# Kernel tuning notes

Hardware: AMD Instinct MI355X
Metric: run time of the kernel (lower is better)

## Reference

```python
import jax, jax.numpy as jnp
import numpy as np

N_NODES = 100000
N_EDGES = 1000000
D_FEAT = 64
N_FILTER = 64
N_CLASSES = 16


def gcn_norm(edge_idx, n):
    """Add self-loops and compute symmetric normalization D^-1/2 (A+I) D^-1/2."""
    loop = jnp.arange(n, dtype=edge_idx.dtype)
    src = jnp.concatenate([edge_idx[0], loop])  # [E+N]
    dst = jnp.concatenate([edge_idx[1], loop])  # [E+N]
    w = jnp.ones(src.shape[0], dtype=jnp.float32)
    deg = jax.ops.segment_sum(w, dst, num_segments=n)  # in-degree incl. self-loop
    dinv = jnp.where(deg > 0, jax.lax.rsqrt(deg), 0.0)
    norm = dinv[src] * w * dinv[dst]  # [E+N]
    return src, dst, norm


def gcn_conv(x, W, b, src, dst, norm, n):
    h = x @ W                                   # [n, f] dense transform first (f <= d)
    msg = h[src] * norm[:, None]                # gather + scale  [E+N, f]
    out = jax.ops.segment_sum(msg, dst, num_segments=n)  # scatter-add  [n, f]
    return out + b


def setup_inputs() -> dict:
    key = jax.random.key(0)
    k1, k2, k3, k4 = jax.random.split(key, 4)
    X = jax.random.normal(k1, (N_NODES, D_FEAT), dtype=jnp.float32)
    edge_idx = jax.random.randint(k2, (2, N_EDGES), 0, N_NODES, dtype=jnp.int64)
    W1 = jax.random.normal(k3, (D_FEAT, N_FILTER), dtype=jnp.float32) * 0.05
    b1 = jnp.zeros((N_FILTER,), dtype=jnp.float32)
    W2 = jax.random.normal(k4, (N_FILTER, N_CLASSES), dtype=jnp.float32) * 0.05
    b2 = jnp.zeros((N_CLASSES,), dtype=jnp.float32)
    return {"X": X, "edge_idx": edge_idx, "W1": W1, "b1": b1, "W2": W2, "b2": b2}


def reference(X, edge_idx, W1, b1, W2, b2):
    n = X.shape[0]
    src, dst, norm = gcn_norm(edge_idx, n)
    x = gcn_conv(X, W1, b1, src, dst, norm, n)
    x = jax.nn.relu(x)
    # dropout p=0 -> identity
    x = gcn_conv(x, W2, b2, src, dst, norm, n)
    return x  # raw logits; pred_layer is not applied in the torch forward
```

## Files before the change

kernel.cpp:

```cpp
#include <hip/hip_runtime.h>
#include <hip/hip_bf16.h>


constexpr int N = 100000;
constexpr int E = 1000000;
constexpr int NB = (N + 511) / 512;
constexpr int CAP = 6144;
constexpr int CSTRIDE = 32;
constexpr int CHUNK = 2048;
constexpr int NBLK = (E + CHUNK - 1) / CHUNK;
constexpr int BT = 512;
constexpr int BTF = 1024;
constexpr int NPW = 3;
constexpr int NW = (N + NPW - 1) / NPW;
constexpr int NWBLK = (NW + 3) / 4;

__device__ __forceinline__ float bflo(unsigned u) { return __uint_as_float(u << 16); }
__device__ __forceinline__ float bfhi(unsigned u) { return __uint_as_float(u & 0xffff0000u); }

__device__ __forceinline__ void wait_lgkm0() {
    __builtin_amdgcn_s_waitcnt(0xc07f);
    __builtin_amdgcn_sched_barrier(0);
}

__global__ void k_bfill(const int* __restrict__ src, const int* __restrict__ dst,
                        int* __restrict__ cursor, int* __restrict__ bkt) {
    __shared__ int hist[256];
    __shared__ int lbase[256];
    __shared__ int gbase[256];
    __shared__ int lcur[256];
    __shared__ int ws[8];
    __shared__ int stage[CHUNK];
    __shared__ unsigned char sbkt[CHUNK];
    int t = threadIdx.x;
    int lane = t & 63;
    int e0 = blockIdx.x * CHUNK;
    int cnt = min(CHUNK, E - e0);

    if (t < 256) hist[t] = 0;
    __syncthreads();
    for (int j = t; j < cnt; j += BT)
        atomicAdd(&hist[dst[e0 + j] >> 9], 1);
    __syncthreads();
    int h = (t < 256) ? hist[t] : 0;
    int v = h;
#pragma unroll
    for (int off = 1; off < 64; off <<= 1) {
        int u = __shfl_up(v, off);
        if (lane >= off) v += u;
    }
    if (lane == 63) ws[t >> 6] = v;
    __syncthreads();
    int add = 0;
    for (int i = 0; i < (t >> 6); ++i) add += ws[i];
    int inc = v + add;
    if (t < 256) { lbase[t] = inc - h; lcur[t] = 0; }
    if (t < NB) gbase[t] = h ? atomicAdd(&cursor[t * CSTRIDE], h) : 0;
    __syncthreads();
    for (int j = t; j < cnt; j += BT) {
        int d = dst[e0 + j];
        int b = d >> 9;
        int pos = lbase[b] + atomicAdd(&lcur[b], 1);
        stage[pos] = ((d & 511) << 17) | src[e0 + j];
        sbkt[pos] = (unsigned char)b;
    }
    __syncthreads();
    for (int j = t; j < cnt; j += BT) {
        int b = sbkt[j];
        int gpos = gbase[b] + (j - lbase[b]);
        if (gpos < CAP) bkt[b * CAP + gpos] = stage[j];
    }
}

__global__ void k_bfine(const int* __restrict__ cursor, const int* __restrict__ bkt,
                        int* __restrict__ row_ptr, float* __restrict__ dinv,
                        int* __restrict__ csr_src) {
    __shared__ int cnt[512];
    __shared__ int excl[512];
    __shared__ int ws[16];
    int b = blockIdx.x;
    int t = threadIdx.x;
    int lane = t & 63;
    int c = (t < NB) ? cursor[t * CSTRIDE] : 0;
    int mv = (t < b) ? c : 0;
#pragma unroll
    for (int off = 1; off < 64; off <<= 1) mv += __shfl_xor(mv, off);
    if (lane == 0) ws[t >> 6] = mv;
    if (t < 512) cnt[t] = 0;
    __syncthreads();
    int base = 0;
#pragma unroll
    for (int i = 0; i < 16; ++i) base += ws[i];
    int m = cursor[b * CSTRIDE];
    if (b == 0 && t == 0) row_ptr[N] = E;
    const int* bb = bkt + b * CAP;
    const int4* bb4 = (const int4*)bb;
    int m4 = m >> 2;
    for (int j = t; j < m4; j += BTF) {
        int4 v = bb4[j];
        atomicAdd(&cnt[v.x >> 17], 1); atomicAdd(&cnt[v.y >> 17], 1);
        atomicAdd(&cnt[v.z >> 17], 1); atomicAdd(&cnt[v.w >> 17], 1);
    }
    for (int j = (m4 << 2) + t; j < m; j += BTF) atomicAdd(&cnt[bb[j] >> 17], 1);
    __syncthreads();
    if (t < 512) {
        int h = cnt[t];
        int v = h;
#pragma unroll
        for (int off = 1; off < 64; off <<= 1) {
            int u = __shfl_up(v, off);
            if (lane >= off) v += u;
        }
        if (lane == 63) ws[t >> 6] = v;
        excl[t] = v - h;
    }
    __syncthreads();
    if (t < 512) {
        int add = 0;
        for (int i = 0; i < (t >> 6); ++i) add += ws[i];
        int ex = excl[t] + add;
        excl[t] = ex;
        int node = b * 512 + t;
        if (node < N) {
            row_ptr[node] = base + ex;
            dinv[node] = rsqrtf((float)(cnt[t] + 1));
        }
    }
    __syncthreads();
    for (int j = t; j < m4; j += BTF) {
        int4 v4 = bb4[j];
        int p0 = atomicAdd(&excl[v4.x >> 17], 1); csr_src[base + p0] = v4.x & 0x1FFFF;
        int p1 = atomicAdd(&excl[v4.y >> 17], 1); csr_src[base + p1] = v4.y & 0x1FFFF;
        int p2 = atomicAdd(&excl[v4.z >> 17], 1); csr_src[base + p2] = v4.z & 0x1FFFF;
        int p3 = atomicAdd(&excl[v4.w >> 17], 1); csr_src[base + p3] = v4.w & 0x1FFFF;
    }
    for (int j = (m4 << 2) + t; j < m; j += BTF) {
        int vv = bb[j];
        int p = atomicAdd(&excl[vv >> 17], 1);
        csr_src[base + p] = vv & 0x1FFFF;
    }
}

__global__ void k_gemm1(const float* __restrict__ X, const float* __restrict__ W1,
                        const float* __restrict__ dinv, __hip_bfloat16* __restrict__ h1s,
                        __hip_bfloat16* __restrict__ h2s) {
    __shared__ float sX[4][4][64];
    int t = threadIdx.x;
    int lane = t & 63;
    int w = t >> 6;
    int wid = (blockIdx.x * 256 + t) >> 6;
    if (blockIdx.x == 0) {
        if (t < 64) h1s[(size_t)N * 64 + t] = __float2bfloat16(0.f);
        if (t < 16) h2s[(size_t)N * 16 + t] = __float2bfloat16(0.f);
    }
    float w1[64];
#pragma unroll
    for (int k = 0; k < 64; ++k) w1[k] = W1[k * 64 + lane];
    constexpr int STRIDE = 4096 * 4;
    int r4 = wid * 4;
    float x0 = X[(size_t)r4 * 64 + lane];
    float x1 = X[(size_t)(r4 + 1) * 64 + lane];
    float x2 = X[(size_t)(r4 + 2) * 64 + lane];
    float x3 = X[(size_t)(r4 + 3) * 64 + lane];
    for (; r4 < N; r4 += STRIDE) {
        int rn = r4 + STRIDE;
        float y0 = 0.f, y1 = 0.f, y2 = 0.f, y3 = 0.f;
        if (rn < N) {
            y0 = X[(size_t)rn * 64 + lane];
            y1 = X[(size_t)(rn + 1) * 64 + lane];
            y2 = X[(size_t)(rn + 2) * 64 + lane];
            y3 = X[(size_t)(rn + 3) * 64 + lane];
        }
        float dv0 = dinv[r4], dv1 = dinv[r4 + 1], dv2 = dinv[r4 + 2], dv3 = dinv[r4 + 3];
        sX[w][0][lane] = x0; sX[w][1][lane] = x1;
        sX[w][2][lane] = x2; sX[w][3][lane] = x3;
        wait_lgkm0();
        float acc0 = 0.f, acc1 = 0.f, acc2 = 0.f, acc3 = 0.f;
#pragma unroll
        for (int k = 0; k < 64; ++k) {
            float wk = w1[k];
            acc0 = fmaf(sX[w][0][k], wk, acc0);
            acc1 = fmaf(sX[w][1][k], wk, acc1);
            acc2 = fmaf(sX[w][2][k], wk, acc2);
            acc3 = fmaf(sX[w][3][k], wk, acc3);
        }
        acc0 *= dv0; acc1 *= dv1; acc2 *= dv2; acc3 *= dv3;
        float up0 = __shfl_xor(acc0, 1);
        float up1 = __shfl_xor(acc1, 1);
        float up2 = __shfl_xor(acc2, 1);
        float up3 = __shfl_xor(acc3, 1);
        if (!(lane & 1)) {
            __hip_bfloat162 p;
            p.x = __float2bfloat16(acc0); p.y = __float2bfloat16(up0);
            *(__hip_bfloat162*)(h1s + (size_t)r4 * 64 + lane) = p;
            p.x = __float2bfloat16(acc1); p.y = __float2bfloat16(up1);
            *(__hip_bfloat162*)(h1s + (size_t)(r4 + 1) * 64 + lane) = p;
            p.x = __float2bfloat16(acc2); p.y = __float2bfloat16(up2);
            *(__hip_bfloat162*)(h1s + (size_t)(r4 + 2) * 64 + lane) = p;
            p.x = __float2bfloat16(acc3); p.y = __float2bfloat16(up3);
            *(__hip_bfloat162*)(h1s + (size_t)(r4 + 3) * 64 + lane) = p;
        }
        x0 = y0; x1 = y1; x2 = y2; x3 = y3;
    }
}

__global__ void k_layer12(const int* __restrict__ row_ptr, const int* __restrict__ csr_src,
                          const float* __restrict__ dinv, const __hip_bfloat16* __restrict__ h1s,
                          const float* __restrict__ b1, const float* __restrict__ W2,
                          __hip_bfloat16* __restrict__ h2s) {
    __shared__ float sy[4][8][72];
    int t = threadIdx.x;
    int lane = t & 63;
    int w = t >> 6;
    int g8 = lane >> 3;
    int qo = (lane & 7) << 4;
    int g16 = lane >> 4, c16 = lane & 15;
    int wid = blockIdx.x * 4 + w;
    int d0 = wid * NPW;
    if (d0 >= N) return;
    int dend = min(d0 + NPW, N);
    float w2[16];
#pragma unroll
    for (int j = 0; j < 16; ++j) w2[j] = W2[(g16 * 16 + j) * 16 + c16];
    float b1v = b1[lane];
    const char* Hb = (const char*)h1s;

    int rp0 = row_ptr[d0];
    for (int d = d0; d < dend; ++d) {
        int rp1 = row_ptr[d + 1];
        float dv = dinv[d];
        float a[8] = {0, 0, 0, 0, 0, 0, 0, 0};
        if (g8 == 0) {
            uint4 u = *(const uint4*)(Hb + (((unsigned)d << 7) | qo));
            a[0] = bflo(u.x); a[1] = bfhi(u.x); a[2] = bflo(u.y); a[3] = bfhi(u.y);
            a[4] = bflo(u.z); a[5] = bfhi(u.z); a[6] = bflo(u.w); a[7] = bfhi(u.w);
        }
        for (int base = rp0; base < rp1; base += 64) {
            int nloc = min(64, rp1 - base);
            int sidx = (lane < nloc) ? csr_src[base + lane] : N;
            int steps = (nloc + 15) >> 4;
            for (int j = 0; j < steps; ++j) {
                int b0 = (j << 4) | g8;
                int s0 = __shfl(sidx, b0);
                int s1 = __shfl(sidx, b0 | 8);
                uint4 u0 = *(const uint4*)(Hb + (((unsigned)s0 << 7) | qo));
                uint4 u1 = *(const uint4*)(Hb + (((unsigned)s1 << 7) | qo));
                a[0] += bflo(u0.x); a[1] += bfhi(u0.x); a[2] += bflo(u0.y); a[3] += bfhi(u0.y);
                a[4] += bflo(u0.z); a[5] += bfhi(u0.z); a[6] += bflo(u0.w); a[7] += bfhi(u0.w);
                a[0] += bflo(u1.x); a[1] += bfhi(u1.x); a[2] += bflo(u1.y); a[3] += bfhi(u1.y);
                a[4] += bflo(u1.z); a[5] += bfhi(u1.z); a[6] += bflo(u1.w); a[7] += bfhi(u1.w);
            }
        }
        rp0 = rp1;
        float* row = &sy[w][g8][(lane & 7) << 3];
        *(float4*)row = make_float4(a[0], a[1], a[2], a[3]);
        *(float4*)(row + 4) = make_float4(a[4], a[5], a[6], a[7]);
        wait_lgkm0();
        float ysum = sy[w][0][lane] + sy[w][1][lane] + sy[w][2][lane] + sy[w][3][lane]
                   + sy[w][4][lane] + sy[w][5][lane] + sy[w][6][lane] + sy[w][7][lane];
        float y = fmaxf(fmaf(dv, ysum, b1v), 0.f);
        float o = 0.f;
#pragma unroll
        for (int j = 0; j < 16; ++j) o = fmaf(__shfl(y, (lane & 48) | j), w2[j], o);
        o += __shfl_xor(o, 16);
        o += __shfl_xor(o, 32);
        o *= dv;
        float oup = __shfl_xor(o, 1);
        if (lane < 16 && !(lane & 1)) {
            __hip_bfloat162 p;
            p.x = __float2bfloat16(o);
            p.y = __float2bfloat16(oup);
            *(__hip_bfloat162*)(h2s + (size_t)d * 16 + lane) = p;
        }
    }
}

__global__ void k_gather2(const int* __restrict__ row_ptr, const int* __restrict__ csr_src,
                          const float* __restrict__ dinv, const __hip_bfloat16* __restrict__ h2s,
                          const float* __restrict__ b2, float* __restrict__ out) {
    int t = threadIdx.x;
    int lane = t & 63;
    int g4 = lane >> 2;
    int q2 = lane & 3;
    int qo = q2 << 3;
    int wid = blockIdx.x * 4 + (t >> 6);
    int d0 = wid * NPW;
    if (d0 >= N) return;
    int dend = min(d0 + NPW, N);
    float b2v[4];
#pragma unroll
    for (int k = 0; k < 4; ++k) b2v[k] = b2[q2 * 4 + k];
    const char* Hb = (const char*)h2s;

    int rp0 = row_ptr[d0];
    for (int d = d0; d < dend; ++d) {
        int rp1 = row_ptr[d + 1];
        float dv = dinv[d];
        float a[4] = {0, 0, 0, 0};
        if (g4 == 0) {
            uint2 u = *(const uint2*)(Hb + (((unsigned)d << 5) | qo));
            a[0] = bflo(u.x); a[1] = bfhi(u.x); a[2] = bflo(u.y); a[3] = bfhi(u.y);
        }
        for (int base = rp0; base < rp1; base += 64) {
            int nloc = min(64, rp1 - base);
            int sidx = (lane < nloc) ? csr_src[base + lane] : N;
            int steps = (nloc + 15) >> 4;
            for (int j = 0; j < steps; ++j) {
                int s = __shfl(sidx, (j << 4) | g4);
                uint2 u = *(const uint2*)(Hb + (((unsigned)s << 5) | qo));
                a[0] += bflo(u.x); a[1] += bfhi(u.x);
                a[2] += bflo(u.y); a[3] += bfhi(u.y);
            }
        }
        rp0 = rp1;
#pragma unroll
        for (int k = 0; k < 4; ++k) {
            a[k] += __shfl_xor(a[k], 4);
            a[k] += __shfl_xor(a[k], 8);
            a[k] += __shfl_xor(a[k], 16);
            a[k] += __shfl_xor(a[k], 32);
        }
        if (lane < 4) {
            float4 r;
            r.x = fmaf(dv, a[0], b2v[0]);
            r.y = fmaf(dv, a[1], b2v[1]);
            r.z = fmaf(dv, a[2], b2v[2]);
            r.w = fmaf(dv, a[3], b2v[3]);
            *(float4*)(out + (size_t)d * 16 + q2 * 4) = r;
        }
    }
}

extern "C" void kernel_launch(void* const* d_in, const int* in_sizes, int n_in,
                              void* d_out, int out_size, void* d_ws, size_t ws_size,
                              hipStream_t stream) {
    const float* X  = (const float*)d_in[0];
    const int*   ei = (const int*)d_in[1];
    const float* W1 = (const float*)d_in[2];
    const float* b1 = (const float*)d_in[3];
    const float* W2 = (const float*)d_in[4];
    const float* b2 = (const float*)d_in[5];
    float* out = (float*)d_out;

    int* cursor  = (int*)d_ws;
    int* row_ptr = cursor + NB * CSTRIDE;
    int* bkt     = row_ptr + N + 4;
    int* csr_src = bkt + NB * CAP;
    float* dinv  = (float*)(csr_src + E);
    __hip_bfloat16* h1s = (__hip_bfloat16*)(dinv + N);
    __hip_bfloat16* h2s = h1s + (size_t)(N + 1) * 64;

    const int* src = ei;
    const int* dst = ei + E;

    hipMemsetAsync(cursor, 0, NB * CSTRIDE * sizeof(int), stream);
    k_bfill<<<NBLK, BT, 0, stream>>>(src, dst, cursor, bkt);
    k_bfine<<<NB, BTF, 0, stream>>>(cursor, bkt, row_ptr, dinv, csr_src);
    k_gemm1<<<1024, 256, 0, stream>>>(X, W1, dinv, h1s, h2s);
    k_layer12<<<NWBLK, 256, 0, stream>>>(row_ptr, csr_src, dinv, h1s, b1, W2, h2s);
    k_gather2<<<NWBLK, 256, 0, stream>>>(row_ptr, csr_src, dinv, h2s, b2, out);
}
```

Baseline: 183.3 us.

## Fuse layer-1 dense transform into CSR build kernel and raise nodes per warp

The separate k_gemm1 launch is removed; each k_bfine block now computes X@W1 for its own 512 nodes after building the CSR rows, scaling by dinv computed from the in-block degree counts. This removes one kernel launch and lets the transform overlap with the CSR build across blocks. In exchange, only 196 blocks (each 1024 threads holding 64 W1 registers under launch_bounds) do the GEMM, so it runs with less parallelism and more register pressure. Separately, nodes per warp in the aggregation kernels rises from 3 to 4.

```diff
diff --git a/kernel.cpp b/kernel.cpp
--- a/kernel.cpp
+++ b/kernel.cpp
@@ -11,7 +11,7 @@
 constexpr int NBLK = (E + CHUNK - 1) / CHUNK;
 constexpr int BT = 512;
 constexpr int BTF = 1024;
-constexpr int NPW = 3;
+constexpr int NPW = 4;
 constexpr int NW = (N + NPW - 1) / NPW;
 constexpr int NWBLK = (NW + 3) / 4;
 
@@ -72,20 +72,32 @@
     }
 }
 
-__global__ void k_bfine(const int* __restrict__ cursor, const int* __restrict__ bkt,
-                        int* __restrict__ row_ptr, float* __restrict__ dinv,
-                        int* __restrict__ csr_src) {
+__global__ __launch_bounds__(1024, 4)
+void k_bfine(const int* __restrict__ cursor, const int* __restrict__ bkt,
+             int* __restrict__ row_ptr, float* __restrict__ dinv,
+             int* __restrict__ csr_src,
+             const float* __restrict__ X, const float* __restrict__ W1,
+             __hip_bfloat16* __restrict__ h1s, __hip_bfloat16* __restrict__ h2s) {
     __shared__ int cnt[512];
     __shared__ int excl[512];
     __shared__ int ws[16];
+    __shared__ float sX[16][4][64];
     int b = blockIdx.x;
     int t = threadIdx.x;
     int lane = t & 63;
+    int wv = t >> 6;
+    float w1r[64];
+#pragma unroll
+    for (int k = 0; k < 64; ++k) w1r[k] = W1[k * 64 + lane];
+    if (b == 0) {
+        if (t < 64) h1s[(size_t)N * 64 + t] = __float2bfloat16(0.f);
+        if (t < 16) h2s[(size_t)N * 16 + t] = __float2bfloat16(0.f);
+    }
     int c = (t < NB) ? cursor[t * CSTRIDE] : 0;
     int mv = (t < b) ? c : 0;
 #pragma unroll
     for (int off = 1; off < 64; off <<= 1) mv += __shfl_xor(mv, off);
-    if (lane == 0) ws[t >> 6] = mv;
+    if (lane == 0) ws[wv] = mv;
     if (t < 512) cnt[t] = 0;
     __syncthreads();
     int base = 0;
@@ -111,13 +123,13 @@
             int u = __shfl_up(v, off);
             if (lane >= off) v += u;
         }
-        if (lane == 63) ws[t >> 6] = v;
+        if (lane == 63) ws[wv] = v;
         excl[t] = v - h;
     }
     __syncthreads();
     if (t < 512) {
         int add = 0;
-        for (int i = 0; i < (t >> 6); ++i) add += ws[i];
+        for (int i = 0; i < wv; ++i) add += ws[i];
         int ex = excl[t] + add;
         excl[t] = ex;
         int node = b * 512 + t;
@@ -139,68 +151,54 @@
         int p = atomicAdd(&excl[vv >> 17], 1);
         csr_src[base + p] = vv & 0x1FFFF;
     }
-}
-
-__global__ void k_gemm1(const float* __restrict__ X, const float* __restrict__ W1,
-                        const float* __restrict__ dinv, __hip_bfloat16* __restrict__ h1s,
-                        __hip_bfloat16* __restrict__ h2s) {
-    __shared__ float sX[4][4][64];
-    int t = threadIdx.x;
-    int lane = t & 63;
-    int w = t >> 6;
-    int wid = (blockIdx.x * 256 + t) >> 6;
-    if (blockIdx.x == 0) {
-        if (t < 64) h1s[(size_t)N * 64 + t] = __float2bfloat16(0.f);
-        if (t < 16) h2s[(size_t)N * 16 + t] = __float2bfloat16(0.f);
-    }
-    float w1[64];
-#pragma unroll
-    for (int k = 0; k < 64; ++k) w1[k] = W1[k * 64 + lane];
-    constexpr int STRIDE = 4096 * 4;
-    int r4 = wid * 4;
-    float x0 = X[(size_t)r4 * 64 + lane];
-    float x1 = X[(size_t)(r4 + 1) * 64 + lane];
-    float x2 = X[(size_t)(r4 + 2) * 64 + lane];
-    float x3 = X[(size_t)(r4 + 3) * 64 + lane];
-    for (; r4 < N; r4 += STRIDE) {
-        int rn = r4 + STRIDE;
-        float y0 = 0.f, y1 = 0.f, y2 = 0.f, y3 = 0.f;
-        if (rn < N) {
-            y0 = X[(size_t)rn * 64 + lane];
-            y1 = X[(size_t)(rn + 1) * 64 + lane];
-            y2 = X[(size_t)(rn + 2) * 64 + lane];
-            y3 = X[(size_t)(rn + 3) * 64 + lane];
-        }
-        float dv0 = dinv[r4], dv1 = dinv[r4 + 1], dv2 = dinv[r4 + 2], dv3 = dinv[r4 + 3];
-        sX[w][0][lane] = x0; sX[w][1][lane] = x1;
-        sX[w][2][lane] = x2; sX[w][3][lane] = x3;
+#pragma unroll 1
+    for (int ch = 0; ch < 8; ++ch) {
+        int r0 = b * 512 + wv * 32 + ch * 4;
+        int lcl = wv * 32 + ch * 4;
+        float x0 = 0.f, x1 = 0.f, x2 = 0.f, x3 = 0.f;
+        if (r0 < N)     x0 = X[(size_t)r0 * 64 + lane];
+        if (r0 + 1 < N) x1 = X[(size_t)(r0 + 1) * 64 + lane];
+        if (r0 + 2 < N) x2 = X[(size_t)(r0 + 2) * 64 + lane];
+        if (r0 + 3 < N) x3 = X[(size_t)(r0 + 3) * 64 + lane];
+        sX[wv][0][lane] = x0; sX[wv][1][lane] = x1;
+        sX[wv][2][lane] = x2; sX[wv][3][lane] = x3;
         wait_lgkm0();
         float acc0 = 0.f, acc1 = 0.f, acc2 = 0.f, acc3 = 0.f;
 #pragma unroll
         for (int k = 0; k < 64; ++k) {
-            float wk = w1[k];
-            acc0 = fmaf(sX[w][0][k], wk, acc0);
-            acc1 = fmaf(sX[w][1][k], wk, acc1);
-            acc2 = fmaf(sX[w][2][k], wk, acc2);
-            acc3 = fmaf(sX[w][3][k], wk, acc3);
-        }
-        acc0 *= dv0; acc1 *= dv1; acc2 *= dv2; acc3 *= dv3;
+            float wk = w1r[k];
+            acc0 = fmaf(sX[wv][0][k], wk, acc0);
+            acc1 = fmaf(sX[wv][1][k], wk, acc1);
+            acc2 = fmaf(sX[wv][2][k], wk, acc2);
+            acc3 = fmaf(sX[wv][3][k], wk, acc3);
+        }
+        acc0 *= rsqrtf((float)(cnt[lcl] + 1));
+        acc1 *= rsqrtf((float)(cnt[lcl + 1] + 1));
+        acc2 *= rsqrtf((float)(cnt[lcl + 2] + 1));
+        acc3 *= rsqrtf((float)(cnt[lcl + 3] + 1));
         float up0 = __shfl_xor(acc0, 1);
         float up1 = __shfl_xor(acc1, 1);
         float up2 = __shfl_xor(acc2, 1);
         float up3 = __shfl_xor(acc3, 1);
         if (!(lane & 1)) {
             __hip_bfloat162 p;
-            p.x = __float2bfloat16(acc0); p.y = __float2bfloat16(up0);
-            *(__hip_bfloat162*)(h1s + (size_t)r4 * 64 + lane) = p;
-            p.x = __float2bfloat16(acc1); p.y = __float2bfloat16(up1);
-            *(__hip_bfloat162*)(h1s + (size_t)(r4 + 1) * 64 + lane) = p;
-            p.x = __float2bfloat16(acc2); p.y = __float2bfloat16(up2);
-            *(__hip_bfloat162*)(h1s + (size_t)(r4 + 2) * 64 + lane) = p;
-            p.x = __float2bfloat16(acc3); p.y = __float2bfloat16(up3);
-            *(__hip_bfloat162*)(h1s + (size_t)(r4 + 3) * 64 + lane) = p;
-        }
-        x0 = y0; x1 = y1; x2 = y2; x3 = y3;
+            if (r0 < N) {
+                p.x = __float2bfloat16(acc0); p.y = __float2bfloat16(up0);
+                *(__hip_bfloat162*)(h1s + (size_t)r0 * 64 + lane) = p;
+            }
+            if (r0 + 1 < N) {
+                p.x = __float2bfloat16(acc1); p.y = __float2bfloat16(up1);
+                *(__hip_bfloat162*)(h1s + (size_t)(r0 + 1) * 64 + lane) = p;
+            }
+            if (r0 + 2 < N) {
+                p.x = __float2bfloat16(acc2); p.y = __float2bfloat16(up2);
+                *(__hip_bfloat162*)(h1s + (size_t)(r0 + 2) * 64 + lane) = p;
+            }
+            if (r0 + 3 < N) {
+                p.x = __float2bfloat16(acc3); p.y = __float2bfloat16(up3);
+                *(__hip_bfloat162*)(h1s + (size_t)(r0 + 3) * 64 + lane) = p;
+            }
+        }
     }
 }
 
@@ -355,8 +353,8 @@
 
     hipMemsetAsync(cursor, 0, NB * CSTRIDE * sizeof(int), stream);
     k_bfill<<<NBLK, BT, 0, stream>>>(src, dst, cursor, bkt);
-    k_bfine<<<NB, BTF, 0, stream>>>(cursor, bkt, row_ptr, dinv, csr_src);
-    k_gemm1<<<1024, 256, 0, stream>>>(X, W1, dinv, h1s, h2s);
+    k_bfine<<<NB, BTF, 0, stream>>>(cursor, bkt, row_ptr, dinv, csr_src,
+                                    X, W1, h1s, h2s);
     k_layer12<<<NWBLK, 256, 0, stream>>>(row_ptr, csr_src, dinv, h1s, b1, W2, h2s);
     k_gather2<<<NWBLK, 256, 0, stream>>>(row_ptr, csr_src, dinv, h2s, b2, out);
 }
```

Result: no change. 186.5 us (+1.8%).
